# Optimization experiments

Measured on AMD Instinct MI355X. Metric: run time of the kernel, lower is better.

## Reference

```python
import jax, jax.numpy as jnp
import numpy as np

N = 50000   # num_entities
R = 16      # num_relations
B = 8       # num_bases
D = 128     # embedding_dim == hidden_dim
E = 625000  # num_edges
EPS = 1e-5  # LayerNorm eps


def _rgcn_layer(x, row, col, edge_type, bases, coef, selfw, bias):
    # weights[r] = sum_b coef[r,b] * bases[b]  (rio). We apply bases to x first
    # (cheaper: N*B*d*d) then mix by coefficients, since (x @ W[r])[col] == x[col] @ W[r].
    z = jnp.einsum('ni,bio->bno', x, bases)          # [B,N,D]
    y = jnp.einsum('rb,bno->rno', coef, z)           # [R,N,D] == x @ W[r]
    msg = y[edge_type, col]                          # [E,D] per-edge messages
    key = edge_type * N + row                        # combined (relation,node) segment id
    agg = jax.ops.segment_sum(msg, key, num_segments=R * N).reshape(R, N, D)
    deg = jax.ops.segment_sum(jnp.ones((msg.shape[0],), x.dtype), key,
                              num_segments=R * N).reshape(R, N, 1)
    agg = (agg / jnp.maximum(deg, 1.0)).sum(0)       # per-relation mean-agg, summed over r
    return x @ selfw + agg + bias


def _layernorm(x, g, b):
    m = x.mean(-1, keepdims=True)
    v = ((x - m) ** 2).mean(-1, keepdims=True)
    return (x - m) * jax.lax.rsqrt(v + EPS) * g + b


def setup_inputs() -> dict:
    key = jax.random.key(0)
    ks = jax.random.split(key, 10)
    s = 1.0 / np.sqrt(D)
    sb = 1.0 / np.sqrt(B)
    return {
        'edge_index': jax.random.randint(ks[0], (2, E), 0, N),
        'edge_type': jax.random.randint(ks[1], (E,), 0, R),
        'emb': jax.random.normal(ks[2], (N, D), jnp.float32) * s,
        'bases1': jax.random.normal(ks[3], (B, D, D), jnp.float32) * s,
        'coef1': jax.random.normal(ks[4], (R, B), jnp.float32) * sb,
        'selfw1': jax.random.normal(ks[5], (D, D), jnp.float32) * s,
        'bias1': jnp.zeros((D,), jnp.float32),
        'g1': jnp.ones((D,), jnp.float32),
        'b1': jnp.zeros((D,), jnp.float32),
        'bases2': jax.random.normal(ks[6], (B, D, D), jnp.float32) * s,
        'coef2': jax.random.normal(ks[7], (R, B), jnp.float32) * sb,
        'selfw2': jax.random.normal(ks[8], (D, D), jnp.float32) * s,
        'bias2': jnp.zeros((D,), jnp.float32),
        'g2': jnp.ones((D,), jnp.float32),
        'b2': jnp.zeros((D,), jnp.float32),
    }


def reference(edge_index, edge_type, emb, bases1, coef1, selfw1, bias1, g1, b1,
              bases2, coef2, selfw2, bias2, g2, b2):
    row, col = edge_index[0], edge_index[1]
    x = emb
    # layer 1 (dropout is identity in eval)
    x = _rgcn_layer(x, row, col, edge_type, bases1, coef1, selfw1, bias1)
    x = jax.nn.relu(_layernorm(x, g1, b1))
    # layer 2
    x = _rgcn_layer(x, row, col, edge_type, bases2, coef2, selfw2, bias2)
    x = jax.nn.relu(_layernorm(x, g2, b2))
    return x
```

## Files before the change

### kernel.cpp

```cpp
#include <hip/hip_runtime.h>
#include <hip/hip_bf16.h>


static constexpr int kDim = 128;
static constexpr int kRel = 16;
static constexpr int kBas = 8;
static constexpr int kSeg = kBas + 1;

typedef __attribute__((ext_vector_type(8))) short bf16x8;
typedef __attribute__((ext_vector_type(4))) float f32x4;

static __device__ __forceinline__ float bf2f_rg(unsigned short h) {
    return __uint_as_float(((unsigned)h) << 16);
}
static __device__ __forceinline__ unsigned short f2bf_rg(float f) {
    unsigned u = __float_as_uint(f);
    u = u + 0x7fffu + ((u >> 16) & 1u);
    return (unsigned short)(u >> 16);
}

static __device__ __forceinline__ void gload_lds16(const void* g, void* l) {
    __builtin_amdgcn_global_load_lds(
        (const __attribute__((address_space(1))) unsigned*)g,
        (__attribute__((address_space(3))) unsigned*)l, 16, 0, 0);
}

static __device__ __forceinline__ int flag_from(const unsigned short* x, int lane) {
    unsigned e0 = ((unsigned)x[lane] >> 7) & 0xFFu;
    unsigned e1 = ((unsigned)x[lane + 64] >> 7) & 0xFFu;
    int bad = (e0 >= 0x86u) || (e1 >= 0x86u);
    return (__ballot(bad) != 0ull) ? 1 : 0;
}

__global__ void RGCNEncoder_89962384982025_kernel(unsigned* p, int n) {
    int i = blockIdx.x * 256 + threadIdx.x;
    if (i < n) p[i] = 0x3F803F80u;
}

__global__ void cvt_rg(const void* xraw, unsigned short* xout, int n) {
    __shared__ int fsh;
    if (threadIdx.x < 64) {
        int fl = flag_from((const unsigned short*)xraw, threadIdx.x);
        if (threadIdx.x == 0) fsh = fl;
    }
    __syncthreads();
    int f = fsh;
    int i = blockIdx.x * 256 + threadIdx.x;
    if (i >= n) return;
    if (f)
        xout[i] = f2bf_rg(((const float*)xraw)[i]);
    else
        xout[i] = ((const unsigned short*)xraw)[i];
}

__global__ void zero_rg(int* p, int n) {
    int i = blockIdx.x * 256 + threadIdx.x;
    if (i < n) p[i] = 0;
}

__global__ void count_rg(const int* ei, const int* et, int* cnt, int E) {
    int e = blockIdx.x * 256 + threadIdx.x;
    if (e < E) atomicAdd(&cnt[ei[e] * kRel + et[e]], 1);
}

__global__ void scanA_rg(const int* cnt, int* rowptr, int* bsum, int n) {
    __shared__ int sh[256];
    int tid = threadIdx.x;
    int i = blockIdx.x * 256 + tid;
    int v = (i < n) ? cnt[i] : 0;
    sh[tid] = v;
    __syncthreads();
    for (int off = 1; off < 256; off <<= 1) {
        int t = (tid >= off) ? sh[tid - off] : 0;
        __syncthreads();
        sh[tid] += t;
        __syncthreads();
    }
    if (i < n) rowptr[i + 1] = sh[tid];
    if (tid == 255) bsum[blockIdx.x] = sh[255];
}
__global__ void scanB_rg(int* bsum, int nb) {
    __shared__ int partial[256];
    int tid = threadIdx.x;
    int chunk = (nb + 255) / 256;
    int s0 = tid * chunk;
    int s1 = min(s0 + chunk, nb);
    int sum = 0;
    for (int i = s0; i < s1; ++i) sum += bsum[i];
    partial[tid] = sum;
    __syncthreads();
    for (int off = 1; off < 256; off <<= 1) {
        int t = (tid >= off) ? partial[tid - off] : 0;
        __syncthreads();
        partial[tid] += t;
        __syncthreads();
    }
    int run = (tid == 0) ? 0 : partial[tid - 1];
    for (int i = s0; i < s1; ++i) { int v = bsum[i]; bsum[i] = run; run += v; }
}
__global__ void scanC_rg(int* rowptr, const int* bsum, int n) {
    int i = blockIdx.x * 256 + threadIdx.x;
    if (i < n) rowptr[i + 1] += bsum[blockIdx.x];
    if (i == 0) rowptr[0] = 0;
}

__global__ void fill_rg(const int* ei, const int* et, const int* rowptr,
                        int* cnt, int* pcols, int E) {
    int e = blockIdx.x * 256 + threadIdx.x;
    if (e < E) {
        int rel = et[e];
        int key = ei[e] * kRel + rel;
        int old = atomicSub(&cnt[key], 1);
        pcols[rowptr[key] + old - 1] = ei[E + e] | (rel << 26);
    }
}

__global__ void wall_rg(const void* bases, const void* coef, const void* selfw,
                        const unsigned short* emb, unsigned short* wallT,
                        float* coefw) {
    __shared__ int fsh;
    if (threadIdx.x < 64) {
        int fl = flag_from(emb, threadIdx.x);
        if (threadIdx.x == 0) fsh = fl;
    }
    __syncthreads();
    int f = fsh;
    int idx = blockIdx.x * 256 + threadIdx.x;
    int b = idx >> 14;
    int o = (idx >> 7) & 127;
    int k = idx & 127;
    if (blockIdx.x == 0 && threadIdx.x < kRel * kBas) {
        coefw[threadIdx.x] = f ? ((const float*)coef)[threadIdx.x]
                               : bf2f_rg(((const unsigned short*)coef)[threadIdx.x]);
    }
    if (b < kBas) {
        float bv = f ? ((const float*)bases)[b * 16384 + k * 128 + o]
                     : bf2f_rg(((const unsigned short*)bases)[b * 16384 + k * 128 + o]);
        wallT[idx] = f2bf_rg(bv);
    } else {
        float sv = f ? ((const float*)selfw)[k * 128 + o]
                     : bf2f_rg(((const unsigned short*)selfw)[k * 128 + o]);
        wallT[idx] = f2bf_rg(sv);
    }
}

__global__ __launch_bounds__(256) void agg2_rg(const int* rowptr2, const int* pcols,
                                               const unsigned short* xsrc,
                                               const float* coefw,
                                               unsigned short* Gall, int N) {
    __shared__ float csh[kRel * kBas];
    if (threadIdx.x < kRel * kBas) csh[threadIdx.x] = coefw[threadIdx.x];
    __syncthreads();
    int wv = threadIdx.x >> 6;
    int lane = threadIdx.x & 63;
    int n = blockIdx.x * 4 + wv;
    if (n >= N) return;
    const int s = rowptr2[n * kRel];
    const int e = rowptr2[n * kRel + kRel];
    const unsigned short* xl = xsrc + 2 * lane;
    float g0[kBas], g1[kBas];
#pragma unroll
    for (int b = 0; b < kBas; ++b) { g0[b] = 0.f; g1[b] = 0.f; }
    float s0 = 0.f, s1 = 0.f;
    int cur = -1, cnt = 0;
    auto flush = [&]() {
        float w = __builtin_amdgcn_rcpf((float)cnt);
        float t0 = s0 * w, t1 = s1 * w;
        const float* cr = csh + cur * kBas;
#pragma unroll
        for (int b = 0; b < kBas; ++b) {
            float c = cr[b];
            g0[b] += c * t0;
            g1[b] += c * t1;
        }
        s0 = 0.f; s1 = 0.f; cnt = 0;
    };
    for (int base = s; base < e; base += 64) {
        int m = e - base;
        if (m > 64) m = 64;
        int pk = 0;
        if (base + lane < e) pk = pcols[base + lane];
        int i = 0;
        for (; i + 4 <= m; i += 4) {
            int v0 = __builtin_amdgcn_readlane(pk, i);
            int v1 = __builtin_amdgcn_readlane(pk, i + 1);
            int v2 = __builtin_amdgcn_readlane(pk, i + 2);
            int v3 = __builtin_amdgcn_readlane(pk, i + 3);
            unsigned u0 = *(const unsigned*)(xl + (size_t)(v0 & 0x03FFFFFF) * 128);
            unsigned u1 = *(const unsigned*)(xl + (size_t)(v1 & 0x03FFFFFF) * 128);
            unsigned u2 = *(const unsigned*)(xl + (size_t)(v2 & 0x03FFFFFF) * 128);
            unsigned u3 = *(const unsigned*)(xl + (size_t)(v3 & 0x03FFFFFF) * 128);
            int r0 = (int)((unsigned)v0 >> 26);
            int r1 = (int)((unsigned)v1 >> 26);
            int r2 = (int)((unsigned)v2 >> 26);
            int r3 = (int)((unsigned)v3 >> 26);
            if (r0 != cur) { if (cnt) flush(); cur = r0; }
            s0 += __uint_as_float(u0 << 16); s1 += __uint_as_float(u0 & 0xffff0000u); ++cnt;
            if (r1 != cur) { flush(); cur = r1; }
            s0 += __uint_as_float(u1 << 16); s1 += __uint_as_float(u1 & 0xffff0000u); ++cnt;
            if (r2 != cur) { flush(); cur = r2; }
            s0 += __uint_as_float(u2 << 16); s1 += __uint_as_float(u2 & 0xffff0000u); ++cnt;
            if (r3 != cur) { flush(); cur = r3; }
            s0 += __uint_as_float(u3 << 16); s1 += __uint_as_float(u3 & 0xffff0000u); ++cnt;
        }
        for (; i < m; ++i) {
            int v = __builtin_amdgcn_readlane(pk, i);
            unsigned u = *(const unsigned*)(xl + (size_t)(v & 0x03FFFFFF) * 128);
            int rel = (int)((unsigned)v >> 26);
            if (rel != cur) { if (cnt) flush(); cur = rel; }
            s0 += __uint_as_float(u << 16);
            s1 += __uint_as_float(u & 0xffff0000u);
            ++cnt;
        }
    }
    if (cnt) flush();
    unsigned short* grow = Gall + (size_t)n * 128 + 2 * lane;
    const size_t plane = (size_t)N * 128;
#pragma unroll
    for (int b = 0; b < kBas; ++b) {
        unsigned outp = (unsigned)f2bf_rg(g0[b]) | ((unsigned)f2bf_rg(g1[b]) << 16);
        *(unsigned*)(grow + (size_t)b * plane) = outp;
    }
}

__global__ __launch_bounds__(256, 3) void fusegemm_rg(const unsigned short* Gall,
                                                      const unsigned short* x,
                                                      const unsigned short* wallT,
                                                      const void* bias, const void* gw,
                                                      const void* bw,
                                                      const unsigned short* emb,
                                                      unsigned short* out_b, float* out_f,
                                                      int ofp32, int M) {
    __shared__ __align__(16) unsigned short As[2][64][128];
    __shared__ float pS[64][5];
    __shared__ float pQ[64][5];
    __shared__ float mrs[64][2];
    __shared__ int fsh;
    const int m0 = blockIdx.x * 64;
    const int tid = threadIdx.x;
    const int wave = tid >> 6;
    const int lane = tid & 63;
    const int wn = wave * 32;
    const int lrow = lane & 15;
    const int lq = lane >> 4;
    if (tid < 64) {
        int fl = flag_from(emb, tid);
        if (tid == 0) fsh = fl;
    }

    auto stage = [&](int seg, int buf) {
        const char* srcb = (seg < kBas)
            ? (const char*)(Gall + (size_t)seg * M * 128)
            : (const char*)x;
#pragma unroll
        for (int it = 0; it < 4; ++it) {
            int gi = (wave * 4 + it) * 64 + lane;
            int row = gi >> 4;
            int c = ((gi & 15) << 4) ^ ((row & 7) << 4);
            int gr = m0 + row;
            if (gr > M - 1) gr = M - 1;
            const char* src = srcb + (size_t)gr * 256 + (size_t)c;
            unsigned short* ldst = &As[buf][0][0] + ((wave * 4 + it) << 9);
            gload_lds16(src, ldst);
        }
    };

    f32x4 acc[4][2] = {};
    stage(0, 0);
    __syncthreads();
    int cur = 0;
    for (int seg = 0; seg < kSeg; ++seg) {
        const unsigned short* Bsrc = wallT + (size_t)seg * 16384;
        bf16x8 b[4][2];
#pragma unroll
        for (int kk4 = 0; kk4 < 4; ++kk4)
#pragma unroll
            for (int nt = 0; nt < 2; ++nt)
                b[kk4][nt] = *(const bf16x8*)(Bsrc + (size_t)(wn + nt * 16 + lrow) * 128
                                              + kk4 * 32 + lq * 8);
        __builtin_amdgcn_sched_barrier(0);
        if (seg < kSeg - 1) stage(seg + 1, cur ^ 1);
#pragma unroll
        for (int kk4 = 0; kk4 < 4; ++kk4) {
            bf16x8 a4[4];
#pragma unroll
            for (int mt = 0; mt < 4; ++mt) {
                int row = mt * 16 + lrow;
                int cb = (kk4 * 64 + lq * 16) ^ ((row & 7) << 4);
                a4[mt] = *(const bf16x8*)((const char*)&As[cur][0][0]
                                          + row * 256 + cb);
            }
#pragma unroll
            for (int mt = 0; mt < 4; ++mt)
#pragma unroll
                for (int nt = 0; nt < 2; ++nt)
                    acc[mt][nt] = __builtin_amdgcn_mfma_f32_16x16x32_bf16(
                        a4[mt], b[kk4][nt], acc[mt][nt], 0, 0, 0);
        }
        asm volatile("s_waitcnt vmcnt(0)" ::: "memory");
        __builtin_amdgcn_s_barrier();
        cur ^= 1;
    }

    const int f = fsh;
    float bv[2], gv[2], betav[2];
#pragma unroll
    for (int nt = 0; nt < 2; ++nt) {
        int gc = wn + nt * 16 + lrow;
        if (f) {
            bv[nt] = ((const float*)bias)[gc];
            gv[nt] = ((const float*)gw)[gc];
            betav[nt] = ((const float*)bw)[gc];
        } else {
            bv[nt] = bf2f_rg(((const unsigned short*)bias)[gc]);
            gv[nt] = bf2f_rg(((const unsigned short*)gw)[gc]);
            betav[nt] = bf2f_rg(((const unsigned short*)bw)[gc]);
        }
    }
#pragma unroll
    for (int mt = 0; mt < 4; ++mt)
#pragma unroll
        for (int i = 0; i < 4; ++i) {
            float sv = 0.f, qv = 0.f;
#pragma unroll
            for (int nt = 0; nt < 2; ++nt) {
                float v = acc[mt][nt][i] + bv[nt];
                acc[mt][nt][i] = v;
                sv += v;
                qv += v * v;
            }
            for (int o = 1; o < 16; o <<= 1) {
                sv += __shfl_xor(sv, o);
                qv += __shfl_xor(qv, o);
            }
            if (lrow == 0) {
                int row = mt * 16 + lq * 4 + i;
                pS[row][wave] = sv;
                pQ[row][wave] = qv;
            }
        }
    __syncthreads();
    if (tid < 64) {
        float s4 = pS[tid][0] + pS[tid][1] + pS[tid][2] + pS[tid][3];
        float q4 = pQ[tid][0] + pQ[tid][1] + pQ[tid][2] + pQ[tid][3];
        float mean = s4 * (1.0f / 128.0f);
        float var = q4 * (1.0f / 128.0f) - mean * mean;
        mrs[tid][0] = mean;
        mrs[tid][1] = rsqrtf(var + 1e-5f);
    }
    __syncthreads();
#pragma unroll
    for (int mt = 0; mt < 4; ++mt)
#pragma unroll
        for (int i = 0; i < 4; ++i) {
            int row = mt * 16 + lq * 4 + i;
            int gr = m0 + row;
            if (gr < M) {
                float mean = mrs[row][0];
                float rs = mrs[row][1];
#pragma unroll
                for (int nt = 0; nt < 2; ++nt) {
                    int gc = wn + nt * 16 + lrow;
                    float o = fmaxf((acc[mt][nt][i] - mean) * rs * gv[nt] + betav[nt], 0.f);
                    if (ofp32)
                        out_f[(size_t)gr * 128 + gc] = o;
                    else
                        out_b[(size_t)gr * 128 + gc] = f2bf_rg(o);
                }
            }
        }
}

extern "C" void kernel_launch(void* const* d_in, const int* in_sizes, int n_in,
                              void* d_out, int out_size, void* d_ws, size_t ws_size,
                              hipStream_t stream) {
    const int* ei = (const int*)d_in[0];
    const int* et = (const int*)d_in[1];
    const void* emb    = d_in[2];
    const void* bases1 = d_in[3];
    const void* coef1  = d_in[4];
    const void* selfw1 = d_in[5];
    const void* bias1  = d_in[6];
    const void* g1     = d_in[7];
    const void* b1     = d_in[8];
    const void* bases2 = d_in[9];
    const void* coef2  = d_in[10];
    const void* selfw2 = d_in[11];
    const void* bias2  = d_in[12];
    const void* g2     = d_in[13];
    const void* b2     = d_in[14];

    const int E = in_sizes[1];
    const int N = out_size / kDim;
    const int n16 = N * kRel;
    const int nsb = (n16 + 255) / 256;

    char* ws = (char*)d_ws;
    size_t off = 0;
    float* coefw = (float*)(ws + off); off += 512;
    int* rowptr2 = (int*)(ws + off); off += (((size_t)n16 + 1) * 4 + 255) & ~(size_t)255;
    int* cnt     = (int*)(ws + off); off += ((size_t)n16 * 4 + 255) & ~(size_t)255;
    int* bsum    = (int*)(ws + off); off += ((size_t)nsb * 4 + 255) & ~(size_t)255;
    int* pcols   = (int*)(ws + off); off += ((size_t)E * 4 + 255) & ~(size_t)255;
    unsigned short* wallT = (unsigned short*)(ws + off);
    off += ((size_t)kSeg * 16384 * 2 + 255) & ~(size_t)255;
    unsigned short* xin  = (unsigned short*)(ws + off);
    off += ((size_t)N * 128 * 2 + 255) & ~(size_t)255;
    unsigned short* xmid = (unsigned short*)(ws + off);
    off += ((size_t)N * 128 * 2 + 255) & ~(size_t)255;
    unsigned short* Gall = (unsigned short*)(ws + off);
    (void)n_in; (void)ws_size;

    const int eblk = (E + 255) / 256;
    const int mblk64 = (N + 63) / 64;
    const int ablk = (N + 3) / 4;
    const int nelem = N * 128;
    const unsigned short* embh = (const unsigned short*)emb;

    RGCNEncoder_89962384982025_kernel<<<1, 256, 0, stream>>>((unsigned*)d_out, 256);

    cvt_rg<<<(nelem + 255) / 256, 256, 0, stream>>>(emb, xin, nelem);

    zero_rg<<<(n16 + 255) / 256, 256, 0, stream>>>(cnt, n16);
    count_rg<<<eblk, 256, 0, stream>>>(ei, et, cnt, E);
    scanA_rg<<<nsb, 256, 0, stream>>>(cnt, rowptr2, bsum, n16);
    scanB_rg<<<1, 256, 0, stream>>>(bsum, nsb);
    scanC_rg<<<nsb, 256, 0, stream>>>(rowptr2, bsum, n16);
    fill_rg<<<eblk, 256, 0, stream>>>(ei, et, rowptr2, cnt, pcols, E);

    wall_rg<<<kSeg * 64, 256, 0, stream>>>(bases1, coef1, selfw1, embh, wallT, coefw);
    agg2_rg<<<ablk, 256, 0, stream>>>(rowptr2, pcols, xin, coefw, Gall, N);
    fusegemm_rg<<<mblk64, 256, 0, stream>>>(Gall, xin, wallT, bias1, g1, b1, embh,
                                            xmid, (float*)nullptr, 0, N);

    wall_rg<<<kSeg * 64, 256, 0, stream>>>(bases2, coef2, selfw2, embh, wallT, coefw);
    agg2_rg<<<ablk, 256, 0, stream>>>(rowptr2, pcols, xmid, coefw, Gall, N);
    fusegemm_rg<<<mblk64, 256, 0, stream>>>(Gall, xmid, wallT, bias2, g2, b2, embh,
                                            (unsigned short*)nullptr, (float*)d_out,
                                            1, N);
}
```

Measured before the change: 374.5 us.

## Load A operands directly from global into registers instead of LDS double-buffer

```diff
diff --git a/kernel.cpp b/kernel.cpp
--- a/kernel.cpp
+++ b/kernel.cpp
@@ -17,12 +17,6 @@
     unsigned u = __float_as_uint(f);
     u = u + 0x7fffu + ((u >> 16) & 1u);
     return (unsigned short)(u >> 16);
-}
-
-static __device__ __forceinline__ void gload_lds16(const void* g, void* l) {
-    __builtin_amdgcn_global_load_lds(
-        (const __attribute__((address_space(1))) unsigned*)g,
-        (__attribute__((address_space(3))) unsigned*)l, 16, 0, 0);
 }
 
 static __device__ __forceinline__ int flag_from(const unsigned short* x, int lane) {
@@ -231,7 +225,6 @@
                                                       const unsigned short* emb,
                                                       unsigned short* out_b, float* out_f,
                                                       int ofp32, int M) {
-    __shared__ __align__(16) unsigned short As[2][64][128];
     __shared__ float pS[64][5];
     __shared__ float pQ[64][5];
     __shared__ float mrs[64][2];
@@ -248,28 +241,20 @@
         if (tid == 0) fsh = fl;
     }
 
-    auto stage = [&](int seg, int buf) {
-        const char* srcb = (seg < kBas)
-            ? (const char*)(Gall + (size_t)seg * M * 128)
-            : (const char*)x;
-#pragma unroll
-        for (int it = 0; it < 4; ++it) {
-            int gi = (wave * 4 + it) * 64 + lane;
-            int row = gi >> 4;
-            int c = ((gi & 15) << 4) ^ ((row & 7) << 4);
-            int gr = m0 + row;
-            if (gr > M - 1) gr = M - 1;
-            const char* src = srcb + (size_t)gr * 256 + (size_t)c;
-            unsigned short* ldst = &As[buf][0][0] + ((wave * 4 + it) << 9);
-            gload_lds16(src, ldst);
-        }
-    };
+    size_t arow[4];
+#pragma unroll
+    for (int mt = 0; mt < 4; ++mt) {
+        int gr = m0 + mt * 16 + lrow;
+        if (gr > M - 1) gr = M - 1;
+        arow[mt] = (size_t)gr * 128 + lq * 8;
+    }
 
     f32x4 acc[4][2] = {};
-    stage(0, 0);
-    __syncthreads();
-    int cur = 0;
+#pragma unroll
     for (int seg = 0; seg < kSeg; ++seg) {
+        const unsigned short* Aseg = (seg < kBas)
+            ? Gall + (size_t)seg * (size_t)M * 128
+            : x;
         const unsigned short* Bsrc = wallT + (size_t)seg * 16384;
         bf16x8 b[4][2];
 #pragma unroll
@@ -278,29 +263,22 @@
             for (int nt = 0; nt < 2; ++nt)
                 b[kk4][nt] = *(const bf16x8*)(Bsrc + (size_t)(wn + nt * 16 + lrow) * 128
                                               + kk4 * 32 + lq * 8);
-        __builtin_amdgcn_sched_barrier(0);
-        if (seg < kSeg - 1) stage(seg + 1, cur ^ 1);
-#pragma unroll
-        for (int kk4 = 0; kk4 < 4; ++kk4) {
-            bf16x8 a4[4];
-#pragma unroll
-            for (int mt = 0; mt < 4; ++mt) {
-                int row = mt * 16 + lrow;
-                int cb = (kk4 * 64 + lq * 16) ^ ((row & 7) << 4);
-                a4[mt] = *(const bf16x8*)((const char*)&As[cur][0][0]
-                                          + row * 256 + cb);
-            }
+        bf16x8 a[4][4];
+#pragma unroll
+        for (int kk4 = 0; kk4 < 4; ++kk4)
+#pragma unroll
+            for (int mt = 0; mt < 4; ++mt)
+                a[kk4][mt] = *(const bf16x8*)(Aseg + arow[mt] + kk4 * 32);
+#pragma unroll
+        for (int kk4 = 0; kk4 < 4; ++kk4)
 #pragma unroll
             for (int mt = 0; mt < 4; ++mt)
 #pragma unroll
                 for (int nt = 0; nt < 2; ++nt)
                     acc[mt][nt] = __builtin_amdgcn_mfma_f32_16x16x32_bf16(
-                        a4[mt], b[kk4][nt], acc[mt][nt], 0, 0, 0);
-        }
-        asm volatile("s_waitcnt vmcnt(0)" ::: "memory");
-        __builtin_amdgcn_s_barrier();
-        cur ^= 1;
-    }
+                        a[kk4][mt], b[kk4][nt], acc[mt][nt], 0, 0, 0);
+    }
+    __syncthreads();
 
     const int f = fsh;
     float bv[2], gv[2], betav[2];
```

New measurement: 482.5 us. +28.8%, slower.

## Retile fused GEMM to 128-row blocks with 8 waves, merge prep launches

Applied to the files above, without the earlier changes.

```diff
diff --git a/kernel.cpp b/kernel.cpp
--- a/kernel.cpp
+++ b/kernel.cpp
@@ -37,7 +37,8 @@
     if (i < n) p[i] = 0x3F803F80u;
 }
 
-__global__ void cvt_rg(const void* xraw, unsigned short* xout, int n) {
+__global__ void prep_rg(const void* xraw, unsigned short* xout, int nelem,
+                        int* cnt, int n16) {
     __shared__ int fsh;
     if (threadIdx.x < 64) {
         int fl = flag_from((const unsigned short*)xraw, threadIdx.x);
@@ -46,16 +47,13 @@
     __syncthreads();
     int f = fsh;
     int i = blockIdx.x * 256 + threadIdx.x;
-    if (i >= n) return;
-    if (f)
-        xout[i] = f2bf_rg(((const float*)xraw)[i]);
-    else
-        xout[i] = ((const unsigned short*)xraw)[i];
-}
-
-__global__ void zero_rg(int* p, int n) {
-    int i = blockIdx.x * 256 + threadIdx.x;
-    if (i < n) p[i] = 0;
+    if (i < n16) cnt[i] = 0;
+    if (i < nelem) {
+        if (f)
+            xout[i] = f2bf_rg(((const float*)xraw)[i]);
+        else
+            xout[i] = ((const unsigned short*)xraw)[i];
+    }
 }
 
 __global__ void count_rg(const int* ei, const int* et, int* cnt, int E) {
@@ -115,9 +113,10 @@
     }
 }
 
-__global__ void wall_rg(const void* bases, const void* coef, const void* selfw,
-                        const unsigned short* emb, unsigned short* wallT,
-                        float* coefw) {
+__global__ void wall2_rg(const void* bases1, const void* coef1, const void* selfw1,
+                         const void* bases2, const void* coef2, const void* selfw2,
+                         const unsigned short* emb, unsigned short* wallT,
+                         float* coefw) {
     __shared__ int fsh;
     if (threadIdx.x < 64) {
         int fl = flag_from(emb, threadIdx.x);
@@ -125,22 +124,30 @@
     }
     __syncthreads();
     int f = fsh;
-    int idx = blockIdx.x * 256 + threadIdx.x;
+    int bi = blockIdx.x;
+    int layer = (bi >= kSeg * 64) ? 1 : 0;
+    int lb = bi - layer * kSeg * 64;
+    const void* bases = layer ? bases2 : bases1;
+    const void* coef  = layer ? coef2  : coef1;
+    const void* selfw = layer ? selfw2 : selfw1;
+    int idx = lb * 256 + threadIdx.x;
     int b = idx >> 14;
     int o = (idx >> 7) & 127;
     int k = idx & 127;
-    if (blockIdx.x == 0 && threadIdx.x < kRel * kBas) {
-        coefw[threadIdx.x] = f ? ((const float*)coef)[threadIdx.x]
-                               : bf2f_rg(((const unsigned short*)coef)[threadIdx.x]);
-    }
+    if (lb == 0 && threadIdx.x < kRel * kBas) {
+        coefw[layer * 128 + threadIdx.x] =
+            f ? ((const float*)coef)[threadIdx.x]
+              : bf2f_rg(((const unsigned short*)coef)[threadIdx.x]);
+    }
+    unsigned short* wout = wallT + (size_t)layer * kSeg * 16384;
     if (b < kBas) {
         float bv = f ? ((const float*)bases)[b * 16384 + k * 128 + o]
                      : bf2f_rg(((const unsigned short*)bases)[b * 16384 + k * 128 + o]);
-        wallT[idx] = f2bf_rg(bv);
+        wout[idx] = f2bf_rg(bv);
     } else {
         float sv = f ? ((const float*)selfw)[k * 128 + o]
                      : bf2f_rg(((const unsigned short*)selfw)[k * 128 + o]);
-        wallT[idx] = f2bf_rg(sv);
+        wout[idx] = f2bf_rg(sv);
     }
 }
 
@@ -223,7 +230,7 @@
     }
 }
 
-__global__ __launch_bounds__(256, 3) void fusegemm_rg(const unsigned short* Gall,
+__global__ __launch_bounds__(512, 4) void fusegemm_rg(const unsigned short* Gall,
                                                       const unsigned short* x,
                                                       const unsigned short* wallT,
                                                       const void* bias, const void* gw,
@@ -231,16 +238,16 @@
                                                       const unsigned short* emb,
                                                       unsigned short* out_b, float* out_f,
                                                       int ofp32, int M) {
-    __shared__ __align__(16) unsigned short As[2][64][128];
-    __shared__ float pS[64][5];
-    __shared__ float pQ[64][5];
-    __shared__ float mrs[64][2];
+    __shared__ __align__(16) unsigned short As[2][128][128];
+    __shared__ float pS[128][8];
+    __shared__ float pQ[128][8];
+    __shared__ float mrs[128][2];
     __shared__ int fsh;
-    const int m0 = blockIdx.x * 64;
+    const int m0 = blockIdx.x * 128;
     const int tid = threadIdx.x;
     const int wave = tid >> 6;
     const int lane = tid & 63;
-    const int wn = wave * 32;
+    const int wn = wave * 16;
     const int lrow = lane & 15;
     const int lq = lane >> 4;
     if (tid < 64) {
@@ -250,52 +257,45 @@
 
     auto stage = [&](int seg, int buf) {
         const char* srcb = (seg < kBas)
-            ? (const char*)(Gall + (size_t)seg * M * 128)
+            ? (const char*)(Gall + (size_t)seg * (size_t)M * 128)
             : (const char*)x;
 #pragma unroll
         for (int it = 0; it < 4; ++it) {
-            int gi = (wave * 4 + it) * 64 + lane;
+            int gi = it * 512 + tid;
             int row = gi >> 4;
             int c = ((gi & 15) << 4) ^ ((row & 7) << 4);
             int gr = m0 + row;
             if (gr > M - 1) gr = M - 1;
             const char* src = srcb + (size_t)gr * 256 + (size_t)c;
-            unsigned short* ldst = &As[buf][0][0] + ((wave * 4 + it) << 9);
+            unsigned short* ldst = &As[buf][0][0] + gi * 8;
             gload_lds16(src, ldst);
         }
     };
 
-    f32x4 acc[4][2] = {};
+    f32x4 acc[8] = {};
     stage(0, 0);
     __syncthreads();
     int cur = 0;
     for (int seg = 0; seg < kSeg; ++seg) {
-        const unsigned short* Bsrc = wallT + (size_t)seg * 16384;
-        bf16x8 b[4][2];
+        const unsigned short* Bsrc = wallT + (size_t)seg * 16384
+                                   + (size_t)(wn + lrow) * 128;
+        bf16x8 b[4];
 #pragma unroll
         for (int kk4 = 0; kk4 < 4; ++kk4)
-#pragma unroll
-            for (int nt = 0; nt < 2; ++nt)
-                b[kk4][nt] = *(const bf16x8*)(Bsrc + (size_t)(wn + nt * 16 + lrow) * 128
-                                              + kk4 * 32 + lq * 8);
+            b[kk4] = *(const bf16x8*)(Bsrc + kk4 * 32 + lq * 8);
         __builtin_amdgcn_sched_barrier(0);
         if (seg < kSeg - 1) stage(seg + 1, cur ^ 1);
 #pragma unroll
         for (int kk4 = 0; kk4 < 4; ++kk4) {
-            bf16x8 a4[4];
-#pragma unroll
-            for (int mt = 0; mt < 4; ++mt) {
+#pragma unroll
+            for (int mt = 0; mt < 8; ++mt) {
                 int row = mt * 16 + lrow;
                 int cb = (kk4 * 64 + lq * 16) ^ ((row & 7) << 4);
-                a4[mt] = *(const bf16x8*)((const char*)&As[cur][0][0]
-                                          + row * 256 + cb);
+                bf16x8 a = *(const bf16x8*)((const char*)&As[cur][0][0]
+                                            + row * 256 + cb);
+                acc[mt] = __builtin_amdgcn_mfma_f32_16x16x32_bf16(
+                    a, b[kk4], acc[mt], 0, 0, 0);
             }
-#pragma unroll
-            for (int mt = 0; mt < 4; ++mt)
-#pragma unroll
-                for (int nt = 0; nt < 2; ++nt)
-                    acc[mt][nt] = __builtin_amdgcn_mfma_f32_16x16x32_bf16(
-                        a4[mt], b[kk4][nt], acc[mt][nt], 0, 0, 0);
         }
         asm volatile("s_waitcnt vmcnt(0)" ::: "memory");
         __builtin_amdgcn_s_barrier();
@@ -303,32 +303,24 @@
     }
 
     const int f = fsh;
-    float bv[2], gv[2], betav[2];
-#pragma unroll
-    for (int nt = 0; nt < 2; ++nt) {
-        int gc = wn + nt * 16 + lrow;
-        if (f) {
-            bv[nt] = ((const float*)bias)[gc];
-            gv[nt] = ((const float*)gw)[gc];
-            betav[nt] = ((const float*)bw)[gc];
-        } else {
-            bv[nt] = bf2f_rg(((const unsigned short*)bias)[gc]);
-            gv[nt] = bf2f_rg(((const unsigned short*)gw)[gc]);
-            betav[nt] = bf2f_rg(((const unsigned short*)bw)[gc]);
-        }
-    }
-#pragma unroll
-    for (int mt = 0; mt < 4; ++mt)
+    const int gc = wn + lrow;
+    float bv, gv, betav;
+    if (f) {
+        bv = ((const float*)bias)[gc];
+        gv = ((const float*)gw)[gc];
+        betav = ((const float*)bw)[gc];
+    } else {
+        bv = bf2f_rg(((const unsigned short*)bias)[gc]);
+        gv = bf2f_rg(((const unsigned short*)gw)[gc]);
+        betav = bf2f_rg(((const unsigned short*)bw)[gc]);
+    }
+#pragma unroll
+    for (int mt = 0; mt < 8; ++mt)
 #pragma unroll
         for (int i = 0; i < 4; ++i) {
-            float sv = 0.f, qv = 0.f;
-#pragma unroll
-            for (int nt = 0; nt < 2; ++nt) {
-                float v = acc[mt][nt][i] + bv[nt];
-                acc[mt][nt][i] = v;
-                sv += v;
-                qv += v * v;
-            }
+            float v = acc[mt][i] + bv;
+            acc[mt][i] = v;
+            float sv = v, qv = v * v;
             for (int o = 1; o < 16; o <<= 1) {
                 sv += __shfl_xor(sv, o);
                 qv += __shfl_xor(qv, o);
@@ -340,33 +332,29 @@
             }
         }
     __syncthreads();
-    if (tid < 64) {
-        float s4 = pS[tid][0] + pS[tid][1] + pS[tid][2] + pS[tid][3];
-        float q4 = pQ[tid][0] + pQ[tid][1] + pQ[tid][2] + pQ[tid][3];
-        float mean = s4 * (1.0f / 128.0f);
-        float var = q4 * (1.0f / 128.0f) - mean * mean;
+    if (tid < 128) {
+        float s8 = 0.f, q8 = 0.f;
+#pragma unroll
+        for (int w = 0; w < 8; ++w) { s8 += pS[tid][w]; q8 += pQ[tid][w]; }
+        float mean = s8 * (1.0f / 128.0f);
+        float var = q8 * (1.0f / 128.0f) - mean * mean;
         mrs[tid][0] = mean;
         mrs[tid][1] = rsqrtf(var + 1e-5f);
     }
     __syncthreads();
 #pragma unroll
-    for (int mt = 0; mt < 4; ++mt)
+    for (int mt = 0; mt < 8; ++mt)
 #pragma unroll
         for (int i = 0; i < 4; ++i) {
             int row = mt * 16 + lq * 4 + i;
             int gr = m0 + row;
             if (gr < M) {
-                float mean = mrs[row][0];
-                float rs = mrs[row][1];
-#pragma unroll
-                for (int nt = 0; nt < 2; ++nt) {
-                    int gc = wn + nt * 16 + lrow;
-                    float o = fmaxf((acc[mt][nt][i] - mean) * rs * gv[nt] + betav[nt], 0.f);
-                    if (ofp32)
-                        out_f[(size_t)gr * 128 + gc] = o;
-                    else
-                        out_b[(size_t)gr * 128 + gc] = f2bf_rg(o);
-                }
+                float o = fmaxf((acc[mt][i] - mrs[row][0]) * mrs[row][1] * gv + betav,
+                                0.f);
+                if (ofp32)
+                    out_f[(size_t)gr * 128 + gc] = o;
+                else
+                    out_b[(size_t)gr * 128 + gc] = f2bf_rg(o);
             }
         }
 }
@@ -397,13 +385,13 @@
 
     char* ws = (char*)d_ws;
     size_t off = 0;
-    float* coefw = (float*)(ws + off); off += 512;
+    float* coefw = (float*)(ws + off); off += 1024;
     int* rowptr2 = (int*)(ws + off); off += (((size_t)n16 + 1) * 4 + 255) & ~(size_t)255;
     int* cnt     = (int*)(ws + off); off += ((size_t)n16 * 4 + 255) & ~(size_t)255;
     int* bsum    = (int*)(ws + off); off += ((size_t)nsb * 4 + 255) & ~(size_t)255;
     int* pcols   = (int*)(ws + off); off += ((size_t)E * 4 + 255) & ~(size_t)255;
     unsigned short* wallT = (unsigned short*)(ws + off);
-    off += ((size_t)kSeg * 16384 * 2 + 255) & ~(size_t)255;
+    off += ((size_t)2 * kSeg * 16384 * 2 + 255) & ~(size_t)255;
     unsigned short* xin  = (unsigned short*)(ws + off);
     off += ((size_t)N * 128 * 2 + 255) & ~(size_t)255;
     unsigned short* xmid = (unsigned short*)(ws + off);
@@ -412,30 +400,32 @@
     (void)n_in; (void)ws_size;
 
     const int eblk = (E + 255) / 256;
-    const int mblk64 = (N + 63) / 64;
+    const int mblk128 = (N + 127) / 128;
     const int ablk = (N + 3) / 4;
     const int nelem = N * 128;
     const unsigned short* embh = (const unsigned short*)emb;
 
     RGCNEncoder_89962384982025_kernel<<<1, 256, 0, stream>>>((unsigned*)d_out, 256);
 
-    cvt_rg<<<(nelem + 255) / 256, 256, 0, stream>>>(emb, xin, nelem);
-
-    zero_rg<<<(n16 + 255) / 256, 256, 0, stream>>>(cnt, n16);
+    prep_rg<<<(nelem + 255) / 256, 256, 0, stream>>>(emb, xin, nelem, cnt, n16);
+
     count_rg<<<eblk, 256, 0, stream>>>(ei, et, cnt, E);
     scanA_rg<<<nsb, 256, 0, stream>>>(cnt, rowptr2, bsum, n16);
     scanB_rg<<<1, 256, 0, stream>>>(bsum, nsb);
     scanC_rg<<<nsb, 256, 0, stream>>>(rowptr2, bsum, n16);
     fill_rg<<<eblk, 256, 0, stream>>>(ei, et, rowptr2, cnt, pcols, E);
 
-    wall_rg<<<kSeg * 64, 256, 0, stream>>>(bases1, coef1, selfw1, embh, wallT, coefw);
+    wall2_rg<<<2 * kSeg * 64, 256, 0, stream>>>(bases1, coef1, selfw1,
+                                                bases2, coef2, selfw2,
+                                                embh, wallT, coefw);
+
     agg2_rg<<<ablk, 256, 0, stream>>>(rowptr2, pcols, xin, coefw, Gall, N);
-    fusegemm_rg<<<mblk64, 256, 0, stream>>>(Gall, xin, wallT, bias1, g1, b1, embh,
-                                            xmid, (float*)nullptr, 0, N);
-
-    wall_rg<<<kSeg * 64, 256, 0, stream>>>(bases2, coef2, selfw2, embh, wallT, coefw);
-    agg2_rg<<<ablk, 256, 0, stream>>>(rowptr2, pcols, xmid, coefw, Gall, N);
-    fusegemm_rg<<<mblk64, 256, 0, stream>>>(Gall, xmid, wallT, bias2, g2, b2, embh,
-                                            (unsigned short*)nullptr, (float*)d_out,
-                                            1, N);
-}
+    fusegemm_rg<<<mblk128, 512, 0, stream>>>(Gall, xin, wallT, bias1, g1, b1, embh,
+                                             xmid, (float*)nullptr, 0, N);
+
+    agg2_rg<<<ablk, 256, 0, stream>>>(rowptr2, pcols, xmid, coefw + 128, Gall, N);
+    fusegemm_rg<<<mblk128, 512, 0, stream>>>(Gall, xmid, wallT + (size_t)kSeg * 16384,
+                                             bias2, g2, b2, embh,
+                                             (unsigned short*)nullptr, (float*)d_out,
+                                             1, N);
+}
```

New measurement: 359.2 us. 1.04x faster.
